# Kernel optimization log

Measured on AMD Instinct MI355X. Metric: run time of the kernel, lower is better.

Reference implementation:

```python
import jax, jax.numpy as jnp
import numpy as np

B, H, N, D = 2, 12, 2048, 64
M = int(D * np.log(D))          # 266 performer random features
E3 = 3 * D                      # performer value hidden size = head_dim*3
DH2 = 2 * D                     # predictor enc hidden = head_dim*2
T = 128                         # attention_predictor_length
CHUNK = 128                     # chunk size for causal linear attention scan
KERNEL_EPS = 1e-3               # performer generalized-kernel epsilon
D_EPS = 1e-6                    # denominator epsilon (added to k_cumsum)
LN_EPS = 1e-5


def setup_inputs() -> dict:
    key = jax.random.key(0)
    ks = jax.random.split(key, 10)
    return {
        "q": jax.random.normal(ks[0], (B, H, N, D), jnp.float32),
        "k": jax.random.normal(ks[1], (B, H, N, D), jnp.float32),
        "v3": jax.random.normal(ks[2], (B, H, N, E3), jnp.float32),
        "proj": jax.random.normal(ks[3], (M, D), jnp.float32),
        "enc_w": jax.random.normal(ks[4], (E3, DH2), jnp.float32) * 0.05,
        "enc_b": jnp.zeros((DH2,), jnp.float32),
        "ln_g": jnp.ones((DH2,), jnp.float32),
        "ln_b": jnp.zeros((DH2,), jnp.float32),
        "dec_w": jax.random.normal(ks[5], (DH2, T), jnp.float32) * 0.05,
        "dec_b": jnp.zeros((T,), jnp.float32),
    }


def _generalized_features(x, proj):
    # performer generalized attention kernel: relu((x / d^0.25) @ proj^T) + eps
    dn = 1.0 / (x.shape[-1] ** 0.25)
    xp = jnp.einsum("bhnd,md->bhnm", x * dn, proj)
    return jax.nn.relu(xp) + KERNEL_EPS


def _causal_linear_attention(qf, kf, v):
    # qf, kf: [B,H,N,M]; v: [B,H,N,E]. Chunked recurrent form of
    # out[n] = (qf[n] . cumsum(kf)[n])^-1 * qf[n] @ cumsum(kf[m] v[m]^T)[n]
    nE = v.shape[-1]
    nc = N // CHUNK
    qc = qf.reshape(B, H, nc, CHUNK, M).transpose(2, 0, 1, 3, 4)
    kc = kf.reshape(B, H, nc, CHUNK, M).transpose(2, 0, 1, 3, 4)
    vc = v.reshape(B, H, nc, CHUNK, nE).transpose(2, 0, 1, 3, 4)
    mask = jnp.tril(jnp.ones((CHUNK, CHUNK), qf.dtype))

    def step(carry, inp):
        ksum, S = carry                      # [B,H,M], [B,H,M,E]
        q_c, k_c, v_c = inp                  # [B,H,C,M], [B,H,C,M], [B,H,C,E]
        qk = jnp.einsum("bhim,bhjm->bhij", q_c, k_c) * mask  # causal within chunk
        # denominator: qf[n] . (k_cumsum[n] + eps)
        d = (jnp.einsum("bhcm,bhm->bhc", q_c, ksum)
             + qk.sum(-1)
             + D_EPS * q_c.sum(-1))
        out = (jnp.einsum("bhcm,bhme->bhce", q_c, S)
               + jnp.einsum("bhij,bhje->bhie", qk, v_c)) / d[..., None]
        ksum = ksum + k_c.sum(axis=2)
        S = S + jnp.einsum("bhcm,bhce->bhme", k_c, v_c)
        return (ksum, S), out

    init = (jnp.zeros((B, H, M), qf.dtype), jnp.zeros((B, H, M, nE), qf.dtype))
    _, outs = jax.lax.scan(step, init, (qc, kc, vc))
    return outs.transpose(1, 2, 0, 3, 4).reshape(B, H, N, nE)


def reference(q, k, v3, proj, enc_w, enc_b, ln_g, ln_b, dec_w, dec_b):
    qf = _generalized_features(q, proj)
    kf = _generalized_features(k, proj)
    ctx = _causal_linear_attention(qf, kf, v3)            # [B,H,N,3D]
    # attention predictor: Linear -> LayerNorm -> GELU -> Linear -> softmax
    h = jnp.einsum("bhne,ec->bhnc", ctx, enc_w) + enc_b    # [B,H,N,2D]
    mu = h.mean(-1, keepdims=True)
    var = ((h - mu) ** 2).mean(-1, keepdims=True)
    h = (h - mu) * jax.lax.rsqrt(var + LN_EPS) * ln_g + ln_b
    h = jax.nn.gelu(h, approximate=False)
    scores = jnp.einsum("bhnc,ct->bhnt", h, dec_w) + dec_b  # [B,H,N,T]
    est_probs = jax.nn.softmax(scores, axis=-1)
    return ctx, est_probs
```

## Files before the change

### kernel.cpp

```cpp
#include <hip/hip_runtime.h>
#include <hip/hip_bf16.h>
#include <math.h>

constexpr int Bn = 2, Hn = 12, BHn = 24;
constexpr int Nn = 2048, Dn = 64;
constexpr int Mn = 266, MPn = 272;
constexpr int E3n = 192, DHn = 128, Tn = 128;
constexpr int Cn = 128, NCn = 16;

#define DNRM 0.35355339059327373f
#define KEPS 1e-3f
#define DEPS 1e-6f
#define LNEPS 1e-5f

static const size_t OFF_QF   = 0;
static const size_t OFF_KF   = 26738688;
static const size_t OFF_QK   = 53477376;
static const size_t OFF_D    = 66060288;
static const size_t OFF_KPRE = 66256896;
static const size_t OFF_S    = 66674688;
static const size_t OFF_WT   = OFF_KF;
static const size_t WS_NEED  = 106782720;

using bf16x8 = __attribute__((ext_vector_type(8))) short;
using f32x4  = __attribute__((ext_vector_type(4))) float;

__device__ inline float u2f(unsigned int u) {
  union { float f; unsigned int i; } c; c.i = u << 16; return c.f;
}
__device__ inline unsigned short f2u(float x) {
  __hip_bfloat16 h = __float2bfloat16(x);
  unsigned short u; __builtin_memcpy(&u, &h, 2); return u;
}
__device__ inline void unpack8(uint4 v, float* a) {
  a[0] = u2f(v.x & 0xffffu); a[1] = u2f(v.x >> 16);
  a[2] = u2f(v.y & 0xffffu); a[3] = u2f(v.y >> 16);
  a[4] = u2f(v.z & 0xffffu); a[5] = u2f(v.z >> 16);
  a[6] = u2f(v.w & 0xffffu); a[7] = u2f(v.w >> 16);
}
__device__ inline ushort4 f4tobf(float4 v) {
  ushort4 o;
  o.x = f2u(v.x); o.y = f2u(v.y); o.z = f2u(v.z); o.w = f2u(v.w);
  return o;
}

__global__ __launch_bounds__(256) void k_features_mfma(
    const float* __restrict__ q, const float* __restrict__ k,
    const float* __restrict__ proj,
    unsigned short* __restrict__ qf, unsigned short* __restrict__ kf) {
  __shared__ unsigned short at[64][40];
  __shared__ unsigned short bt[272][40];
  const float* x = (blockIdx.y == 0) ? q : k;
  unsigned short* outp = (blockIdx.y == 0) ? qf : kf;
  int tid = threadIdx.x;
  int w = tid >> 6, l = tid & 63;
  int l16 = l & 15, lg = l >> 4;
  int r0 = blockIdx.x * 64;

  f32x4 acc[17] = {};
  for (int kt = 0; kt < 2; ++kt) {
    int k0 = kt * 32;
    __syncthreads();
    #pragma unroll
    for (int p = 0; p < 2; ++p) {
      int idx = tid + p * 256;
      int row = idx >> 3, kq = idx & 7;
      float4 v = *(const float4*)(x + (size_t)(r0 + row) * Dn + k0 + kq * 4);
      *(ushort4*)&at[row][kq * 4] = f4tobf(v);
    }
    for (int idx = tid; idx < 2176; idx += 256) {
      int mq = idx >> 3, kq = idx & 7;
      float4 v = make_float4(0.f, 0.f, 0.f, 0.f);
      if (mq < Mn) v = *(const float4*)(proj + (size_t)mq * Dn + k0 + kq * 4);
      *(ushort4*)&bt[mq][kq * 4] = f4tobf(v);
    }
    __syncthreads();
    bf16x8 a = *(const bf16x8*)((const char*)&at[0][0] + (w*16 + l16) * 80 + lg * 16);
    #pragma unroll
    for (int ct = 0; ct < 17; ++ct) {
      bf16x8 b = *(const bf16x8*)((const char*)&bt[0][0] + (ct*16 + l16) * 80 + lg * 16);
      acc[ct] = __builtin_amdgcn_mfma_f32_16x16x32_bf16(a, b, acc[ct], 0, 0, 0);
    }
  }
  #pragma unroll
  for (int ct = 0; ct < 17; ++ct)
    #pragma unroll
    for (int reg = 0; reg < 4; ++reg) {
      int row = r0 + w*16 + lg*4 + reg;
      int m = ct*16 + l16;
      float val = 0.f;
      if (m < Mn) val = fmaxf(acc[ct][reg] * DNRM, 0.f) + KEPS;
      outp[(size_t)row * MPn + m] = f2u(val);
    }
}

__global__ __launch_bounds__(256) void k_ksum(const unsigned short* __restrict__ kf,
                                              float* __restrict__ kpre) {
  int blk = blockIdx.x; int bh = blk >> 4, c = blk & 15;
  int tid = threadIdx.x;
  for (int m = tid; m < MPn; m += 256) {
    const unsigned short* base = kf + ((size_t)bh * Nn + (size_t)c * Cn) * MPn + m;
    float s = 0.f;
    #pragma unroll 8
    for (int j = 0; j < Cn; ++j) s += u2f(base[(size_t)j * MPn]);
    kpre[((size_t)bh * NCn + c) * MPn + m] = s;
  }
}

__global__ __launch_bounds__(256) void k_kprefix(float* __restrict__ kpre) {
  int bh = blockIdx.x; int tid = threadIdx.x;
  for (int m = tid; m < MPn; m += 256) {
    float v[NCn];
    #pragma unroll
    for (int c = 0; c < NCn; ++c) v[c] = kpre[((size_t)bh * NCn + c) * MPn + m];
    float acc = 0.f;
    #pragma unroll
    for (int c = 0; c < NCn; ++c) {
      kpre[((size_t)bh * NCn + c) * MPn + m] = acc;
      acc += v[c];
    }
  }
}

__global__ __launch_bounds__(256) void k_qk_mfma(
    const unsigned short* __restrict__ qf,
    const unsigned short* __restrict__ kf,
    const float* __restrict__ kpre,
    unsigned short* __restrict__ qkout,
    float* __restrict__ dden) {
  __shared__ unsigned short at[128][40];
  __shared__ unsigned short ktl[128][40];
  __shared__ float kp[MPn];
  __shared__ float rs_lds[128];
  int blk = blockIdx.x;
  int bh = blk >> 4, c = blk & 15;
  int tid = threadIdx.x;
  int w = tid >> 6, l = tid & 63;
  int l16 = l & 15, lg = l >> 4;
  size_t qbase = ((size_t)bh * Nn + (size_t)c * Cn) * MPn;
  size_t rbase = (size_t)bh * Nn + (size_t)c * Cn;
  for (int m = tid; m < MPn; m += 256) kp[m] = kpre[((size_t)bh * NCn + c) * MPn + m];

  f32x4 acc[2][8] = {};
  for (int kt = 0; kt < 9; ++kt) {
    int mt = kt * 32;
    __syncthreads();
    #pragma unroll
    for (int p = 0; p < 2; ++p) {
      int idx = tid * 8 + p * 2048;
      int r = idx >> 5, kk = idx & 31;
      uint4 va = make_uint4(0u,0u,0u,0u), vk = make_uint4(0u,0u,0u,0u);
      if (mt + kk < MPn) {
        va = *(const uint4*)(qf + qbase + (size_t)r * MPn + mt + kk);
        vk = *(const uint4*)(kf + qbase + (size_t)r * MPn + mt + kk);
      }
      *(uint4*)((char*)&at[0][0] + r * 80 + kk * 2) = va;
      *(uint4*)((char*)&ktl[0][0] + r * 80 + kk * 2) = vk;
    }
    __syncthreads();
    bf16x8 a0 = *(const bf16x8*)((const char*)&at[0][0] + (w*32 + l16) * 80 + lg * 16);
    bf16x8 a1 = *(const bf16x8*)((const char*)&at[0][0] + (w*32 + 16 + l16) * 80 + lg * 16);
    #pragma unroll
    for (int ct = 0; ct < 8; ++ct) {
      bf16x8 b = *(const bf16x8*)((const char*)&ktl[0][0] + (ct*16 + l16) * 80 + lg * 16);
      acc[0][ct] = __builtin_amdgcn_mfma_f32_16x16x32_bf16(a0, b, acc[0][ct], 0, 0, 0);
      acc[1][ct] = __builtin_amdgcn_mfma_f32_16x16x32_bf16(a1, b, acc[1][ct], 0, 0, 0);
    }
  }
  size_t qkbase = (size_t)blk * (Cn * Cn);
  float rs[2][4] = {};
  #pragma unroll
  for (int rt = 0; rt < 2; ++rt)
    #pragma unroll
    for (int ct = 0; ct < 8; ++ct)
      #pragma unroll
      for (int reg = 0; reg < 4; ++reg) {
        int row = w*32 + rt*16 + lg*4 + reg;
        int col = ct*16 + l16;
        float v = (col <= row) ? acc[rt][ct][reg] : 0.f;
        qkout[qkbase + (size_t)row * Cn + col] = f2u(v);
        rs[rt][reg] += v;
      }
  #pragma unroll
  for (int rt = 0; rt < 2; ++rt)
    #pragma unroll
    for (int reg = 0; reg < 4; ++reg) {
      float s = rs[rt][reg];
      s += __shfl_xor(s, 1); s += __shfl_xor(s, 2);
      s += __shfl_xor(s, 4); s += __shfl_xor(s, 8);
      rs[rt][reg] = s;
    }
  if (l16 == 0) {
    #pragma unroll
    for (int rt = 0; rt < 2; ++rt)
      #pragma unroll
      for (int reg = 0; reg < 4; ++reg)
        rs_lds[w*32 + rt*16 + lg*4 + reg] = rs[rt][reg];
  }
  __syncthreads();
  if (tid < 128) {
    float dot = 0.f, qs = 0.f;
    const unsigned short* qrow = qf + qbase + (size_t)tid * MPn;
    for (int m = 0; m < MPn; m += 8) {
      uint4 v = *(const uint4*)(qrow + m);
      float a[8]; unpack8(v, a);
      #pragma unroll
      for (int t = 0; t < 8; ++t) { dot += a[t] * kp[m + t]; qs += a[t]; }
    }
    dden[rbase + tid] = rs_lds[tid] + dot + DEPS * qs;
  }
}

__global__ __launch_bounds__(256) void k_schunk_mfma(
    const unsigned short* __restrict__ kf,
    const float* __restrict__ v3,
    unsigned short* __restrict__ ST) {
  __shared__ unsigned short at[64][40];
  __shared__ unsigned short bt[272][40];
  int blk = blockIdx.x, ey = blockIdx.y;
  int bh = blk >> 4, c = blk & 15;
  int e0 = ey * 64;
  int tid = threadIdx.x;
  int w = tid >> 6, l = tid & 63;
  int l16 = l & 15, lg = l >> 4;
  size_t vbase = ((size_t)bh * Nn + (size_t)c * Cn) * E3n + e0;
  size_t kbase = ((size_t)bh * Nn + (size_t)c * Cn) * MPn;

  f32x4 acc[17] = {};
  for (int kt = 0; kt < 4; ++kt) {
    int jt = kt * 32;
    __syncthreads();
    #pragma unroll
    for (int p = 0; p < 2; ++p) {
      int idx = tid + p * 256;
      int j = idx & 31, eq = idx >> 5;
      float4 v = *(const float4*)(v3 + vbase + (size_t)(jt + j) * E3n + eq * 4);
      at[eq*4+0][j] = f2u(v.x); at[eq*4+1][j] = f2u(v.y);
      at[eq*4+2][j] = f2u(v.z); at[eq*4+3][j] = f2u(v.w);
    }
    for (int idx = tid; idx < 1088; idx += 256) {
      int j = idx & 31, mq = idx >> 5;
      uint4 v = *(const uint4*)(kf + kbase + (size_t)(jt + j) * MPn + mq * 8);
      unsigned short tmp[8]; __builtin_memcpy(tmp, &v, 16);
      #pragma unroll
      for (int t = 0; t < 8; ++t) bt[mq*8+t][j] = tmp[t];
    }
    __syncthreads();
    bf16x8 a = *(const bf16x8*)((const char*)&at[0][0] + (w*16 + l16) * 80 + lg * 16);
    #pragma unroll
    for (int ct = 0; ct < 17; ++ct) {
      bf16x8 b = *(const bf16x8*)((const char*)&bt[0][0] + (ct*16 + l16) * 80 + lg * 16);
      acc[ct] = __builtin_amdgcn_mfma_f32_16x16x32_bf16(a, b, acc[ct], 0, 0, 0);
    }
  }
  size_t stbase = (size_t)blk * MPn * E3n + (size_t)e0 * MPn;
  #pragma unroll
  for (int ct = 0; ct < 17; ++ct)
    #pragma unroll
    for (int reg = 0; reg < 4; ++reg) {
      int e_loc = w*16 + lg*4 + reg;
      ST[stbase + (size_t)e_loc * MPn + ct*16 + l16] = f2u(acc[ct][reg]);
    }
}

__global__ __launch_bounds__(256) void k_wt(const float* __restrict__ enc_w,
    const float* __restrict__ dec_w, unsigned short* __restrict__ ewt,
    unsigned short* __restrict__ dwt) {
  int i = blockIdx.x * 256 + threadIdx.x;
  if (i < 128 * 192) {
    int n = i / 192, e = i - n * 192;
    ewt[i] = f2u(enc_w[(size_t)e * DHn + n]);
  } else {
    int j = i - 128 * 192;
    int t = j >> 7, c = j & 127;
    dwt[(size_t)t * DHn + c] = f2u(dec_w[(size_t)c * Tn + t]);
  }
}

__global__ __launch_bounds__(256) void k_sprefix(unsigned short* __restrict__ S) {
  int bh = blockIdx.x / 51, sub = blockIdx.x % 51;
  int idx4 = sub * 256 + threadIdx.x;
  size_t off = (size_t)idx4 * 4;
  ushort4 v[NCn];
  #pragma unroll
  for (int c = 0; c < NCn; ++c)
    v[c] = *(const ushort4*)(S + ((size_t)(bh * NCn + c)) * MPn * E3n + off);
  float a0 = 0.f, a1 = 0.f, a2 = 0.f, a3 = 0.f;
  #pragma unroll
  for (int c = 0; c < NCn; ++c) {
    ushort4 o;
    unsigned short* op = (unsigned short*)&o;
    op[0] = f2u(a0); op[1] = f2u(a1); op[2] = f2u(a2); op[3] = f2u(a3);
    *(ushort4*)(S + ((size_t)(bh * NCn + c)) * MPn * E3n + off) = o;
    a0 += u2f(v[c].x); a1 += u2f(v[c].y); a2 += u2f(v[c].z); a3 += u2f(v[c].w);
  }
}

__global__ __launch_bounds__(256) void k_ctx_mfma(
    const unsigned short* __restrict__ qf,
    const unsigned short* __restrict__ qkm,
    const unsigned short* __restrict__ ST,
    const float* __restrict__ v3,
    const float* __restrict__ dden,
    float* __restrict__ ctx) {
  __shared__ unsigned short at[128][40];
  __shared__ unsigned short bt[64][40];
  __shared__ float dd[128];
  int blk = blockIdx.x, ey = blockIdx.y;
  int bh = blk >> 4, c = blk & 15;
  int e0 = ey * 64;
  int tid = threadIdx.x;
  int w = tid >> 6, l = tid & 63;
  int l16 = l & 15, lg = l >> 4;
  size_t qbase = ((size_t)bh * Nn + (size_t)c * Cn) * MPn;
  size_t sbase = (size_t)blk * MPn * E3n + (size_t)e0 * MPn;
  size_t rbase = (size_t)bh * Nn + (size_t)c * Cn;
  if (tid < 128) dd[tid] = dden[rbase + tid];

  f32x4 acc[2][4] = {};
  for (int kt = 0; kt < 9; ++kt) {
    int mt = kt * 32;
    __syncthreads();
    #pragma unroll
    for (int p = 0; p < 2; ++p) {
      int idx = tid * 8 + p * 2048;
      int r = idx >> 5, kk = idx & 31;
      uint4 v = make_uint4(0u,0u,0u,0u);
      if (mt + kk < MPn) v = *(const uint4*)(qf + qbase + (size_t)r * MPn + mt + kk);
      *(uint4*)((char*)&at[0][0] + r * 80 + kk * 2) = v;
    }
    {
      int r = tid >> 2, kk = (tid & 3) * 8;
      uint4 v = make_uint4(0u,0u,0u,0u);
      if (mt + kk < MPn) v = *(const uint4*)(ST + sbase + (size_t)r * MPn + mt + kk);
      *(uint4*)((char*)&bt[0][0] + r * 80 + kk * 2) = v;
    }
    __syncthreads();
    bf16x8 a0 = *(const bf16x8*)((const char*)&at[0][0] + (w*32 + l16) * 80 + lg * 16);
    bf16x8 a1 = *(const bf16x8*)((const char*)&at[0][0] + (w*32 + 16 + l16) * 80 + lg * 16);
    #pragma unroll
    for (int ct = 0; ct < 4; ++ct) {
      bf16x8 b = *(const bf16x8*)((const char*)&bt[0][0] + (ct*16 + l16) * 80 + lg * 16);
      acc[0][ct] = __builtin_amdgcn_mfma_f32_16x16x32_bf16(a0, b, acc[0][ct], 0, 0, 0);
      acc[1][ct] = __builtin_amdgcn_mfma_f32_16x16x32_bf16(a1, b, acc[1][ct], 0, 0, 0);
    }
  }
  size_t kkbase = (size_t)blk * (Cn * Cn);
  size_t vb3 = ((size_t)bh * Nn + (size_t)c * Cn) * E3n + e0;
  for (int kt = 0; kt < 4; ++kt) {
    int jt = kt * 32;
    __syncthreads();
    #pragma unroll
    for (int p = 0; p < 2; ++p) {
      int idx = tid * 8 + p * 2048;
      int r = idx >> 5, kk = idx & 31;
      uint4 v = *(const uint4*)(qkm + kkbase + (size_t)r * Cn + jt + kk);
      *(uint4*)((char*)&at[0][0] + r * 80 + kk * 2) = v;
    }
    #pragma unroll
    for (int p = 0; p < 2; ++p) {
      int idx = tid + p * 256;
      int j = idx & 31, eq = idx >> 5;
      float4 v = *(const float4*)(v3 + vb3 + (size_t)(jt + j) * E3n + eq * 4);
      bt[eq*4+0][j] = f2u(v.x); bt[eq*4+1][j] = f2u(v.y);
      bt[eq*4+2][j] = f2u(v.z); bt[eq*4+3][j] = f2u(v.w);
    }
    __syncthreads();
    bf16x8 a0 = *(const bf16x8*)((const char*)&at[0][0] + (w*32 + l16) * 80 + lg * 16);
    bf16x8 a1 = *(const bf16x8*)((const char*)&at[0][0] + (w*32 + 16 + l16) * 80 + lg * 16);
    #pragma unroll
    for (int ct = 0; ct < 4; ++ct) {
      bf16x8 b = *(const bf16x8*)((const char*)&bt[0][0] + (ct*16 + l16) * 80 + lg * 16);
      acc[0][ct] = __builtin_amdgcn_mfma_f32_16x16x32_bf16(a0, b, acc[0][ct], 0, 0, 0);
      acc[1][ct] = __builtin_amdgcn_mfma_f32_16x16x32_bf16(a1, b, acc[1][ct], 0, 0, 0);
    }
  }
  #pragma unroll
  for (int rt = 0; rt < 2; ++rt)
    #pragma unroll
    for (int ct = 0; ct < 4; ++ct)
      #pragma unroll
      for (int reg = 0; reg < 4; ++reg) {
        int row = w*32 + rt*16 + lg*4 + reg;
        float inv = 1.f / dd[row];
        ctx[(rbase + row) * (size_t)E3n + e0 + ct*16 + l16] = acc[rt][ct][reg] * inv;
      }
}

__global__ __launch_bounds__(256) void k_pred_fused(
    const float* __restrict__ ctx,
    const unsigned short* __restrict__ ewt,
    const unsigned short* __restrict__ dwt,
    const float* __restrict__ enc_b, const float* __restrict__ ln_g,
    const float* __restrict__ ln_b, const float* __restrict__ dec_b,
    float* __restrict__ probs) {
  __shared__ unsigned short at[128][40];
  __shared__ unsigned short bt[128][40];
  __shared__ unsigned short ht[128][200];
  int tid = threadIdx.x;
  int w = tid >> 6, l = tid & 63;
  int l16 = l & 15, lg = l >> 4;
  size_t r0 = (size_t)blockIdx.x * 128;

  float ebv[8], ggv[8], llv[8], dbv[8];
  #pragma unroll
  for (int ct = 0; ct < 8; ++ct) {
    ebv[ct] = enc_b[ct*16 + l16];
    ggv[ct] = ln_g[ct*16 + l16];
    llv[ct] = ln_b[ct*16 + l16];
    dbv[ct] = dec_b[ct*16 + l16];
  }

  f32x4 acc1[2][8] = {};
  for (int kt = 0; kt < 6; ++kt) {
    int k0 = kt * 32;
    __syncthreads();
    #pragma unroll
    for (int p = 0; p < 4; ++p) {
      int idx = tid + p * 256;
      int row = idx >> 3, kq = idx & 7;
      float4 v = *(const float4*)(ctx + (r0 + row) * E3n + k0 + kq * 4);
      *(ushort4*)&at[row][kq * 4] = f4tobf(v);
    }
    #pragma unroll
    for (int p = 0; p < 2; ++p) {
      int idx = tid + p * 256;
      int n = idx >> 2, kq = idx & 3;
      *(uint4*)&bt[n][kq * 8] = *(const uint4*)(ewt + (size_t)n * E3n + k0 + kq * 8);
    }
    __syncthreads();
    bf16x8 a0 = *(const bf16x8*)((const char*)&at[0][0] + (w*32 + l16) * 80 + lg * 16);
    bf16x8 a1 = *(const bf16x8*)((const char*)&at[0][0] + (w*32 + 16 + l16) * 80 + lg * 16);
    #pragma unroll
    for (int ct = 0; ct < 8; ++ct) {
      bf16x8 b = *(const bf16x8*)((const char*)&bt[0][0] + (ct*16 + l16) * 80 + lg * 16);
      acc1[0][ct] = __builtin_amdgcn_mfma_f32_16x16x32_bf16(a0, b, acc1[0][ct], 0, 0, 0);
      acc1[1][ct] = __builtin_amdgcn_mfma_f32_16x16x32_bf16(a1, b, acc1[1][ct], 0, 0, 0);
    }
  }
  #pragma unroll
  for (int rt = 0; rt < 2; ++rt) {
    #pragma unroll
    for (int reg = 0; reg < 4; ++reg) {
      float hv[8];
      float s = 0.f, s2 = 0.f;
      #pragma unroll
      for (int ct = 0; ct < 8; ++ct) {
        float v = acc1[rt][ct][reg] + ebv[ct];
        hv[ct] = v; s += v; s2 += v * v;
      }
      #pragma unroll
      for (int m = 1; m < 16; m <<= 1) { s += __shfl_xor(s, m); s2 += __shfl_xor(s2, m); }
      float mu = s * (1.f / 128.f);
      float var = s2 * (1.f / 128.f) - mu * mu;
      float rsq = rsqrtf(var + LNEPS);
      int row = w*32 + rt*16 + lg*4 + reg;
      #pragma unroll
      for (int ct = 0; ct < 8; ++ct) {
        float v = (hv[ct] - mu) * rsq * ggv[ct] + llv[ct];
        v = 0.5f * v * (1.f + erff(v * 0.70710678118654752f));
        ht[row][ct*16 + l16] = f2u(v);
      }
    }
  }
  f32x4 acc2[2][8] = {};
  for (int kt = 0; kt < 4; ++kt) {
    int c0 = kt * 32;
    __syncthreads();
    #pragma unroll
    for (int p = 0; p < 2; ++p) {
      int idx = tid + p * 256;
      int t = idx >> 2, kq = idx & 3;
      *(uint4*)&bt[t][kq * 8] = *(const uint4*)(dwt + (size_t)t * DHn + c0 + kq * 8);
    }
    __syncthreads();
    bf16x8 a0 = *(const bf16x8*)&ht[w*32 + l16][c0 + lg*8];
    bf16x8 a1 = *(const bf16x8*)&ht[w*32 + 16 + l16][c0 + lg*8];
    #pragma unroll
    for (int ct = 0; ct < 8; ++ct) {
      bf16x8 b = *(const bf16x8*)((const char*)&bt[0][0] + (ct*16 + l16) * 80 + lg * 16);
      acc2[0][ct] = __builtin_amdgcn_mfma_f32_16x16x32_bf16(a0, b, acc2[0][ct], 0, 0, 0);
      acc2[1][ct] = __builtin_amdgcn_mfma_f32_16x16x32_bf16(a1, b, acc2[1][ct], 0, 0, 0);
    }
  }
  #pragma unroll
  for (int rt = 0; rt < 2; ++rt) {
    #pragma unroll
    for (int reg = 0; reg < 4; ++reg) {
      float sv[8];
      float m = -1e30f;
      #pragma unroll
      for (int ct = 0; ct < 8; ++ct) {
        sv[ct] = acc2[rt][ct][reg] + dbv[ct];
        m = fmaxf(m, sv[ct]);
      }
      #pragma unroll
      for (int mm = 1; mm < 16; mm <<= 1) m = fmaxf(m, __shfl_xor(m, mm));
      float s = 0.f;
      #pragma unroll
      for (int ct = 0; ct < 8; ++ct) { sv[ct] = expf(sv[ct] - m); s += sv[ct]; }
      #pragma unroll
      for (int mm = 1; mm < 16; mm <<= 1) s += __shfl_xor(s, mm);
      float inv = 1.f / s;
      int row = w*32 + rt*16 + lg*4 + reg;
      #pragma unroll
      for (int ct = 0; ct < 8; ++ct)
        probs[(r0 + row) * (size_t)Tn + ct*16 + l16] = sv[ct] * inv;
    }
  }
}

extern "C" void kernel_launch(void* const* d_in, const int* in_sizes, int n_in,
                              void* d_out, int out_size, void* d_ws, size_t ws_size,
                              hipStream_t stream) {
  const float* q     = (const float*)d_in[0];
  const float* k     = (const float*)d_in[1];
  const float* v3    = (const float*)d_in[2];
  const float* proj  = (const float*)d_in[3];
  const float* enc_w = (const float*)d_in[4];
  const float* enc_b = (const float*)d_in[5];
  const float* ln_g  = (const float*)d_in[6];
  const float* ln_b  = (const float*)d_in[7];
  const float* dec_w = (const float*)d_in[8];
  const float* dec_b = (const float*)d_in[9];
  float* out = (float*)d_out;
  char* ws = (char*)d_ws;
  if (ws_size < WS_NEED) return;

  unsigned short* qf   = (unsigned short*)(ws + OFF_QF);
  unsigned short* kf   = (unsigned short*)(ws + OFF_KF);
  unsigned short* qk   = (unsigned short*)(ws + OFF_QK);
  float*          dden = (float*)(ws + OFF_D);
  float*          kpre = (float*)(ws + OFF_KPRE);
  unsigned short* ST   = (unsigned short*)(ws + OFF_S);
  unsigned short* ewt  = (unsigned short*)(ws + OFF_WT);
  unsigned short* dwt  = (unsigned short*)(ws + OFF_WT + 49152);
  float* ctx   = out;
  float* probs = out + (size_t)BHn * Nn * E3n;

  k_features_mfma<<<dim3(BHn * Nn / 64, 2), 256, 0, stream>>>(q, k, proj, qf, kf);
  k_ksum        <<<dim3(BHn * NCn),     256, 0, stream>>>(kf, kpre);
  k_kprefix     <<<dim3(BHn),           256, 0, stream>>>(kpre);
  k_qk_mfma     <<<dim3(BHn * NCn),     256, 0, stream>>>(qf, kf, kpre, qk, dden);
  k_schunk_mfma <<<dim3(BHn * NCn, 3),  256, 0, stream>>>(kf, v3, ST);
  k_wt          <<<dim3(160),           256, 0, stream>>>(enc_w, dec_w, ewt, dwt);
  k_sprefix     <<<dim3(BHn * 51),      256, 0, stream>>>(ST);
  k_ctx_mfma    <<<dim3(BHn * NCn, 3),  256, 0, stream>>>(qf, qk, ST, v3, dden, ctx);
  k_pred_fused  <<<dim3(BHn * Nn / 128),256, 0, stream>>>(ctx, ewt, dwt, enc_b, ln_g,
                                                          ln_b, dec_b, probs);
}
```

Baseline: 168.7 us.

## Fuse per-chunk key sums into state-chunk kernel and retile its E dimension

Removes the separate k_ksum kernel by computing the per-chunk column sums of the key features from the LDS tile already staged in k_schunk_mfma (only the ey==0 blocks do this). The state-chunk kernel moves from 3 blocks of 256 threads over E to 2 blocks of 384 threads covering 96 columns each, so the key tile is loaded twice per chunk instead of three times. Global-to-LDS staging of v3 and kf changes from vectorised float4/uint4 loads to scalar element loads, and the v3 staging in k_ctx_mfma changes the same way. This saves one launch and some key-tile traffic, at the cost of less vectorised and possibly less coalesced memory access.

Result: slower. 182.4 us (+8.1%).

```diff
diff --git a/kernel.cpp b/kernel.cpp
--- a/kernel.cpp
+++ b/kernel.cpp
@@ -92,19 +92,6 @@
       if (m < Mn) val = fmaxf(acc[ct][reg] * DNRM, 0.f) + KEPS;
       outp[(size_t)row * MPn + m] = f2u(val);
     }
-}
-
-__global__ __launch_bounds__(256) void k_ksum(const unsigned short* __restrict__ kf,
-                                              float* __restrict__ kpre) {
-  int blk = blockIdx.x; int bh = blk >> 4, c = blk & 15;
-  int tid = threadIdx.x;
-  for (int m = tid; m < MPn; m += 256) {
-    const unsigned short* base = kf + ((size_t)bh * Nn + (size_t)c * Cn) * MPn + m;
-    float s = 0.f;
-    #pragma unroll 8
-    for (int j = 0; j < Cn; ++j) s += u2f(base[(size_t)j * MPn]);
-    kpre[((size_t)bh * NCn + c) * MPn + m] = s;
-  }
 }
 
 __global__ __launch_bounds__(256) void k_kprefix(float* __restrict__ kpre) {
@@ -211,15 +198,16 @@
   }
 }
 
-__global__ __launch_bounds__(256) void k_schunk_mfma(
+__global__ __launch_bounds__(384) void k_schunk_mfma(
     const unsigned short* __restrict__ kf,
     const float* __restrict__ v3,
-    unsigned short* __restrict__ ST) {
-  __shared__ unsigned short at[64][40];
+    unsigned short* __restrict__ ST,
+    float* __restrict__ kpre) {
+  __shared__ unsigned short at[96][40];
   __shared__ unsigned short bt[272][40];
   int blk = blockIdx.x, ey = blockIdx.y;
   int bh = blk >> 4, c = blk & 15;
-  int e0 = ey * 64;
+  int e0 = ey * 96;
   int tid = threadIdx.x;
   int w = tid >> 6, l = tid & 63;
   int l16 = l & 15, lg = l >> 4;
@@ -227,23 +215,19 @@
   size_t kbase = ((size_t)bh * Nn + (size_t)c * Cn) * MPn;
 
   f32x4 acc[17] = {};
+  float ks = 0.f;
   for (int kt = 0; kt < 4; ++kt) {
     int jt = kt * 32;
     __syncthreads();
     #pragma unroll
-    for (int p = 0; p < 2; ++p) {
-      int idx = tid + p * 256;
-      int j = idx & 31, eq = idx >> 5;
-      float4 v = *(const float4*)(v3 + vbase + (size_t)(jt + j) * E3n + eq * 4);
-      at[eq*4+0][j] = f2u(v.x); at[eq*4+1][j] = f2u(v.y);
-      at[eq*4+2][j] = f2u(v.z); at[eq*4+3][j] = f2u(v.w);
-    }
-    for (int idx = tid; idx < 1088; idx += 256) {
-      int j = idx & 31, mq = idx >> 5;
-      uint4 v = *(const uint4*)(kf + kbase + (size_t)(jt + j) * MPn + mq * 8);
-      unsigned short tmp[8]; __builtin_memcpy(tmp, &v, 16);
-      #pragma unroll
-      for (int t = 0; t < 8; ++t) bt[mq*8+t][j] = tmp[t];
+    for (int p = 0; p < 8; ++p) {
+      int idx = tid + p * 384;
+      int e = idx % 96, j = idx / 96;
+      at[e][j] = f2u(v3[vbase + (size_t)(jt + j) * E3n + e]);
+    }
+    for (int idx = tid; idx < 8704; idx += 384) {
+      int m = idx % 272, j = idx / 272;
+      bt[m][j] = kf[kbase + (size_t)(jt + j) * MPn + m];
     }
     __syncthreads();
     bf16x8 a = *(const bf16x8*)((const char*)&at[0][0] + (w*16 + l16) * 80 + lg * 16);
@@ -252,6 +236,15 @@
       bf16x8 b = *(const bf16x8*)((const char*)&bt[0][0] + (ct*16 + l16) * 80 + lg * 16);
       acc[ct] = __builtin_amdgcn_mfma_f32_16x16x32_bf16(a, b, acc[ct], 0, 0, 0);
     }
+    if (ey == 0 && tid < MPn) {
+      #pragma unroll
+      for (int jq = 0; jq < 4; ++jq) {
+        uint4 v = *(const uint4*)((const char*)&bt[0][0] + tid * 80 + jq * 16);
+        float a8[8]; unpack8(v, a8);
+        #pragma unroll
+        for (int t = 0; t < 8; ++t) ks += a8[t];
+      }
+    }
   }
   size_t stbase = (size_t)blk * MPn * E3n + (size_t)e0 * MPn;
   #pragma unroll
@@ -261,6 +254,8 @@
       int e_loc = w*16 + lg*4 + reg;
       ST[stbase + (size_t)e_loc * MPn + ct*16 + l16] = f2u(acc[ct][reg]);
     }
+  if (ey == 0 && tid < MPn)
+    kpre[((size_t)bh * NCn + c) * MPn + tid] = ks;
 }
 
 __global__ __launch_bounds__(256) void k_wt(const float* __restrict__ enc_w,
@@ -358,12 +353,10 @@
       *(uint4*)((char*)&at[0][0] + r * 80 + kk * 2) = v;
     }
     #pragma unroll
-    for (int p = 0; p < 2; ++p) {
+    for (int p = 0; p < 8; ++p) {
       int idx = tid + p * 256;
-      int j = idx & 31, eq = idx >> 5;
-      float4 v = *(const float4*)(v3 + vb3 + (size_t)(jt + j) * E3n + eq * 4);
-      bt[eq*4+0][j] = f2u(v.x); bt[eq*4+1][j] = f2u(v.y);
-      bt[eq*4+2][j] = f2u(v.z); bt[eq*4+3][j] = f2u(v.w);
+      int e = idx & 63, j = idx >> 6;
+      bt[e][j] = f2u(v3[vb3 + (size_t)j * E3n + e]);
     }
     __syncthreads();
     bf16x8 a0 = *(const bf16x8*)((const char*)&at[0][0] + (w*32 + l16) * 80 + lg * 16);
@@ -374,6 +367,7 @@
       acc[0][ct] = __builtin_amdgcn_mfma_f32_16x16x32_bf16(a0, b, acc[0][ct], 0, 0, 0);
       acc[1][ct] = __builtin_amdgcn_mfma_f32_16x16x32_bf16(a1, b, acc[1][ct], 0, 0, 0);
     }
+    vb3 += 32 * E3n;
   }
   #pragma unroll
   for (int rt = 0; rt < 2; ++rt)
@@ -539,10 +533,9 @@
   float* probs = out + (size_t)BHn * Nn * E3n;
 
   k_features_mfma<<<dim3(BHn * Nn / 64, 2), 256, 0, stream>>>(q, k, proj, qf, kf);
-  k_ksum        <<<dim3(BHn * NCn),     256, 0, stream>>>(kf, kpre);
+  k_schunk_mfma <<<dim3(BHn * NCn, 2),  384, 0, stream>>>(kf, v3, ST, kpre);
   k_kprefix     <<<dim3(BHn),           256, 0, stream>>>(kpre);
   k_qk_mfma     <<<dim3(BHn * NCn),     256, 0, stream>>>(qf, kf, kpre, qk, dden);
-  k_schunk_mfma <<<dim3(BHn * NCn, 3),  256, 0, stream>>>(kf, v3, ST);
   k_wt          <<<dim3(160),           256, 0, stream>>>(enc_w, dec_w, ewt, dwt);
   k_sprefix     <<<dim3(BHn * 51),      256, 0, stream>>>(ST);
   k_ctx_mfma    <<<dim3(BHn * NCn, 3),  256, 0, stream>>>(qf, qk, ST, v3, dden, ctx);
```
